# Kernel optimization log

Hardware: AMD Instinct MI355X
Metric: run time of the kernel (lower is better)

## Reference

```python
import jax, jax.numpy as jnp
import numpy as np

N1, N2, D = 2048, 2048, 64  # d_q_in=d_q_out=d_k_in=d_k_out=d_v=64


def setup_inputs() -> dict:
    key = jax.random.key(0)
    ks = jax.random.split(key, 9)
    s = 0.05
    return {
        "q": jax.random.normal(ks[0], (N1, D), dtype=jnp.float32),
        "k": jax.random.normal(ks[1], (N2, D), dtype=jnp.float32),
        "v": jax.random.normal(ks[2], (N2, D), dtype=jnp.float32),
        # q_w: Linear(d_q_in -> d_q_out)
        "Wq": jax.random.normal(ks[3], (D, D), dtype=jnp.float32) * s,
        "bq": jax.random.normal(ks[4], (D,), dtype=jnp.float32) * s,
        # k_w: Linear(d_k_in -> d_k_out)
        "Wk": jax.random.normal(ks[5], (D, D), dtype=jnp.float32) * s,
        "bk": jax.random.normal(ks[6], (D,), dtype=jnp.float32) * s,
        # w: Linear(d_q_out -> 1)
        "w": jax.random.normal(ks[7], (D,), dtype=jnp.float32) * s,
        "b": jax.random.normal(ks[8], (1,), dtype=jnp.float32) * s,
    }


def reference(q, k, v, Wq, bq, Wk, bk, w, b):
    # x' = w3 * sigma(w1*q + w2*k); Bahdanau-style additive attention.
    qp = q @ Wq + bq                      # [N1, D]
    kp = k @ Wk + bk                      # [N2, D]
    h = jax.nn.sigmoid(qp[:, None, :] + kp[None, :, :])   # [N1, N2, D]
    att_score = jnp.einsum("nmd,d->nm", h, w) + b[0]       # [N1, N2]
    att_weight = jax.nn.softmax(att_score, axis=-1)
    output = att_weight @ v               # [N1, D]
    return (output, att_score)
```

## Files before the change

### kernel.cpp

```cpp
#include <hip/hip_runtime.h>
#include <math.h>

#define N1 2048
#define N2 2048
#define DD 64
#define NJ 10
#define KDIM (DD*NJ)
#define NKS32 40

static constexpr float LOG2E = 1.4426950408889634f;
static constexpr float ACLIP = 2.6f;

typedef _Float16 f16x8  __attribute__((ext_vector_type(8)));
typedef float    f32x16 __attribute__((ext_vector_type(16)));
typedef float    v2f    __attribute__((ext_vector_type(2)));

__device__ const float XNODE_dev[NJ] = {
     2.5679897f,  2.3166170f,  1.8384776f,  1.1803753f,  0.4067296f,
    -0.4067296f, -1.1803753f, -1.8384776f, -2.3166170f, -2.5679897f };
__device__ const float WBAR_dev[NJ] = {
     1.4751660e-3f, -4.2811330e-3f,  6.6679880e-3f, -8.4021590e-3f,
     9.3138610e-3f, -9.3138610e-3f,  8.4021590e-3f, -6.6679880e-3f,
     4.2811330e-3f, -1.4751660e-3f };

__device__ __forceinline__ void gll16(const void* g, void* l) {
    __builtin_amdgcn_global_load_lds(
        (const __attribute__((address_space(1))) void*)g,
        (__attribute__((address_space(3))) void*)l,
        16, 0, 0);
}

__global__ __launch_bounds__(256) void k_prep(
    const float* __restrict__ q, const float* __restrict__ k,
    const float* __restrict__ Wq, const float* __restrict__ bq,
    const float* __restrict__ Wk, const float* __restrict__ bk,
    const float* __restrict__ w,
    f16x8* __restrict__ Ap, f16x8* __restrict__ Bp)
{
    int t = threadIdx.x;
    bool is_q = blockIdx.x < 64;
    int tile = is_q ? blockIdx.x : (blockIdx.x - 64);
    int row0 = tile * 32;
    const float* X    = is_q ? q : k;
    const float* W    = is_q ? Wq : Wk;
    const float* bias = is_q ? bq : bk;

    __shared__ float4 xs4[32][16];
    __shared__ float  pp[32][66];
    __shared__ float  wls[64];
    __shared__ float  xn_s[NJ], wb_s[NJ];

    #pragma unroll
    for (int s = 0; s < 2; ++s) {
        int slot = t + 256 * s;
        int r = slot >> 4, c4 = slot & 15;
        xs4[r][c4] = *(const float4*)&X[(row0 + r) * DD + c4 * 4];
    }
    if (t < 64) wls[t] = w[t];
    if (t >= 64 && t < 64 + NJ) xn_s[t - 64] = XNODE_dev[t - 64];
    if (t >= 96 && t < 96 + NJ) wb_s[t - 96] = WBAR_dev[t - 96];
    __syncthreads();

    {
        int col = t & 63, wvi = t >> 6;
        float acc[8];
        float bv = bias[col];
        #pragma unroll
        for (int i = 0; i < 8; ++i) acc[i] = bv;
        #pragma unroll
        for (int j4 = 0; j4 < 16; ++j4) {
            float wj[4];
            #pragma unroll
            for (int jj = 0; jj < 4; ++jj)
                wj[jj] = W[(j4 * 4 + jj) * DD + col];
            #pragma unroll
            for (int i = 0; i < 8; ++i) {
                float4 xv = xs4[wvi + 4 * i][j4];
                acc[i] = fmaf(xv.x, wj[0], acc[i]);
                acc[i] = fmaf(xv.y, wj[1], acc[i]);
                acc[i] = fmaf(xv.z, wj[2], acc[i]);
                acc[i] = fmaf(xv.w, wj[3], acc[i]);
            }
        }
        #pragma unroll
        for (int i = 0; i < 8; ++i)
            pp[wvi + 4 * i][col] = acc[i];
    }
    __syncthreads();

    #pragma unroll
    for (int s = 0; s < 10; ++s) {
        int slot = t + 256 * s;
        int ks = slot >> 6, lane = slot & 63;
        int row = lane & 31;
        int kbase = ks * 16 + (lane >> 5) * 8;
        f16x8 o;
        if (is_q) {
            #pragma unroll
            for (int jj = 0; jj < 8; ++jj) {
                int kk = kbase + jj;
                int d = (kk * 6554) >> 16;
                int j = kk - d * 10;
                float a = pp[row][d];
                a = fminf(fmaxf(a, -ACLIP), ACLIP);
                float p = wb_s[j];
                #pragma unroll
                for (int i = 0; i < NJ; ++i)
                    p *= (i == j) ? 1.0f : (a - xn_s[i]);
                o[jj] = (_Float16)(p * wls[d]);
            }
            Ap[(tile * NKS32 + ks) * 64 + lane] = o;
        } else {
            #pragma unroll
            for (int jj = 0; jj < 8; ++jj) {
                int kk = kbase + jj;
                int d = (kk * 6554) >> 16;
                int j = kk - d * 10;
                float sv = xn_s[j] + pp[row][d];
                float sg = __builtin_amdgcn_rcpf(
                    1.0f + __builtin_amdgcn_exp2f(-sv * LOG2E));
                o[jj] = (_Float16)sg;
            }
            Bp[(tile * NKS32 + ks) * 64 + lane] = o;
        }
    }
}

__global__ __launch_bounds__(256) void k_gemm(
    const f16x8* __restrict__ Ap, const f16x8* __restrict__ Bp,
    const float* __restrict__ bscal, float* __restrict__ score)
{
    int bx = blockIdx.x;
    int xcd = bx & 7;
    int sub = (bx >> 3) & 3;
    int mb  = bx >> 5;
    int nb  = xcd * 4 + sub;

    int t = threadIdx.x, wv = t >> 6, lane = t & 63;
    int ma = (wv >> 1) * 2;
    int nloc = wv & 1;

    __shared__ f16x8 sbuf[24][64];

    const int ST = NKS32 * 64;

    const f16x8* cbase[6];
    int ckl[6];
    #pragma unroll
    for (int j = 0; j < 6; ++j) {
        int cc = wv * 6 + j;
        int tile = cc >> 2;
        ckl[j] = cc & 3;
        cbase[j] = (tile < 4) ? (Ap + (mb * 4 + tile) * ST)
                              : (Bp + (nb * 2 + (tile - 4)) * ST);
    }

    f32x16 acc[2] = {};

    for (int it = 0; it < 10; ++it) {
        if (it) __syncthreads();
        #pragma unroll
        for (int j = 0; j < 6; ++j) {
            int cc = wv * 6 + j;
            gll16(cbase[j] + (it * 4 + ckl[j]) * 64 + lane, &sbuf[cc][0]);
        }
        __syncthreads();
        #pragma unroll
        for (int kl = 0; kl < 4; ++kl) {
            f16x8 a0 = sbuf[(ma + 0) * 4 + kl][lane];
            f16x8 a1 = sbuf[(ma + 1) * 4 + kl][lane];
            f16x8 b  = sbuf[(4 + nloc) * 4 + kl][lane];
            acc[0] = __builtin_amdgcn_mfma_f32_32x32x16_f16(a0, b, acc[0], 0, 0, 0);
            acc[1] = __builtin_amdgcn_mfma_f32_32x32x16_f16(a1, b, acc[1], 0, 0, 0);
        }
    }

    float bias = bscal[0];
    int nt0 = nb * 2 + nloc;
    int colg = nt0 * 32 + (lane & 31);
    #pragma unroll
    for (int i = 0; i < 2; ++i) {
        int rbase = (mb * 4 + ma + i) * 32 + 4 * (lane >> 5);
        #pragma unroll
        for (int r = 0; r < 16; ++r) {
            int rowg = rbase + (r & 3) + 8 * (r >> 2);
            score[rowg * N2 + colg] = acc[i][r] + bias;
        }
    }
}

__global__ __launch_bounds__(256) void k_out(
    const float* __restrict__ score, const float* __restrict__ v,
    float* __restrict__ out)
{
    int n0 = blockIdx.x * 4;
    __shared__ float p_lds[2][2048][2];
    __shared__ float red[4][4];
    __shared__ float part[4][4][64];
    __shared__ float inv_s[4];
    int t = threadIdx.x, wv = t >> 6, lane = t & 63;

    float psum[4];
    #pragma unroll
    for (int r = 0; r < 4; ++r) {
        psum[r] = 0.f;
        const float* srow = score + (n0 + r) * N2;
        #pragma unroll
        for (int kk = 0; kk < 8; ++kk) {
            int m = t + 256 * kk;
            float p = __builtin_amdgcn_exp2f(srow[m] * LOG2E);
            p_lds[r >> 1][m][r & 1] = p;
            psum[r] += p;
        }
    }
    #pragma unroll
    for (int r = 0; r < 4; ++r) {
        float x = psum[r];
        #pragma unroll
        for (int off = 32; off > 0; off >>= 1)
            x += __shfl_down(x, off, 64);
        if (lane == 0) red[r][wv] = x;
    }
    __syncthreads();
    if (t < 4)
        inv_s[t] = 1.0f / (red[t][0] + red[t][1] + red[t][2] + red[t][3]);
    __syncthreads();

    int m_off = lane >> 4, d4 = lane & 15;
    const float4* v4 = (const float4*)v;
    float4 a[4] = {{0,0,0,0},{0,0,0,0},{0,0,0,0},{0,0,0,0}};
    int mstart = wv * 512;
    #pragma unroll 4
    for (int i = 0; i < 128; ++i) {
        int m = mstart + i * 4 + m_off;
        v2f p01 = *(const v2f*)&p_lds[0][m][0];
        v2f p23 = *(const v2f*)&p_lds[1][m][0];
        float4 vv = v4[m * 16 + d4];
        a[0].x = fmaf(p01.x, vv.x, a[0].x);  a[0].y = fmaf(p01.x, vv.y, a[0].y);
        a[0].z = fmaf(p01.x, vv.z, a[0].z);  a[0].w = fmaf(p01.x, vv.w, a[0].w);
        a[1].x = fmaf(p01.y, vv.x, a[1].x);  a[1].y = fmaf(p01.y, vv.y, a[1].y);
        a[1].z = fmaf(p01.y, vv.z, a[1].z);  a[1].w = fmaf(p01.y, vv.w, a[1].w);
        a[2].x = fmaf(p23.x, vv.x, a[2].x);  a[2].y = fmaf(p23.x, vv.y, a[2].y);
        a[2].z = fmaf(p23.x, vv.z, a[2].z);  a[2].w = fmaf(p23.x, vv.w, a[2].w);
        a[3].x = fmaf(p23.y, vv.x, a[3].x);  a[3].y = fmaf(p23.y, vv.y, a[3].y);
        a[3].z = fmaf(p23.y, vv.z, a[3].z);  a[3].w = fmaf(p23.y, vv.w, a[3].w);
    }
    #pragma unroll
    for (int r = 0; r < 4; ++r) {
        #pragma unroll
        for (int off = 16; off <= 32; off <<= 1) {
            a[r].x += __shfl_xor(a[r].x, off, 64);
            a[r].y += __shfl_xor(a[r].y, off, 64);
            a[r].z += __shfl_xor(a[r].z, off, 64);
            a[r].w += __shfl_xor(a[r].w, off, 64);
        }
    }
    if (lane < 16) {
        #pragma unroll
        for (int r = 0; r < 4; ++r)
            *(float4*)&part[wv][r][d4 * 4] = a[r];
    }
    __syncthreads();
    {
        int r = t >> 6, d = t & 63;
        float s = part[0][r][d] + part[1][r][d] + part[2][r][d] + part[3][r][d];
        out[(n0 + r) * DD + d] = s * inv_s[r];
    }
}

__global__ __launch_bounds__(256) void k_proj_old(
    const float* __restrict__ q, const float* __restrict__ k,
    const float* __restrict__ Wq, const float* __restrict__ bq,
    const float* __restrict__ Wk, const float* __restrict__ bk,
    float* __restrict__ qp, float* __restrict__ kpT)
{
    int bx = blockIdx.x;
    bool is_q = bx < 512;
    int row0 = (is_q ? bx : bx - 512) * 4;
    const float* X = is_q ? q : k;
    const float* W = is_q ? Wq : Wk;
    const float* bias = is_q ? bq : bk;

    __shared__ float xrow[4][64];
    int t = threadIdx.x;
    int wv = t >> 6, lane = t & 63;
    xrow[wv][lane] = X[(row0 + wv) * DD + lane];
    __syncthreads();

    float acc = 0.f;
    #pragma unroll
    for (int j = 0; j < 64; ++j)
        acc = fmaf(xrow[wv][j], W[j * DD + lane], acc);

    float val = -(acc + bias[lane]) * LOG2E;
    int row = row0 + wv;
    if (is_q) qp[row * DD + lane] = val;
    else      kpT[lane * N2 + row] = val;
}

__global__ __launch_bounds__(256, 8) void k_score_old(
    const float* __restrict__ qp, const float* __restrict__ kpT,
    const float* __restrict__ w, const float* __restrict__ b,
    float* __restrict__ score)
{
    int bx = blockIdx.x;
    int n0 = (bx >> 3) * 8;
    int m_base = (bx & 7) * 256;

    __shared__ float qp_s[8][64];
    __shared__ float w_s[64];
    int t = threadIdx.x;
    if (t < 128)
        ((float4*)qp_s)[t] = ((const float4*)(qp + n0 * DD))[t];
    if (t < 64) w_s[t] = w[t];
    float b0 = b[0];
    __syncthreads();

    int rgrp = t >> 6, lane = t & 63;
    int r0 = rgrp * 2;
    int m0 = m_base + lane * 4;

    float acc[2][4];
    #pragma unroll
    for (int i2 = 0; i2 < 2; ++i2)
        #pragma unroll
        for (int j = 0; j < 4; ++j)
            acc[i2][j] = b0;

    const float* kbase = kpT + m0;

    for (int d0 = 0; d0 < 64; d0 += 4) {
        float4 kv[4];
        #pragma unroll
        for (int dd = 0; dd < 4; ++dd)
            kv[dd] = *(const float4*)(kbase + (d0 + dd) * N2);

        float4 wvv = *(const float4*)&w_s[d0];
        #pragma unroll
        for (int i2 = 0; i2 < 2; ++i2) {
            float4 qv = *(const float4*)&qp_s[r0 + i2][d0];
            #pragma unroll
            for (int dd = 0; dd < 4; ++dd) {
                float qvd = (&qv.x)[dd];
                float wd  = (&wvv.x)[dd];
                #pragma unroll
                for (int j = 0; j < 4; ++j) {
                    float x = qvd + (&kv[dd].x)[j];
                    float e = __builtin_amdgcn_exp2f(x);
                    float sg = __builtin_amdgcn_rcpf(1.0f + e);
                    acc[i2][j] = fmaf(wd, sg, acc[i2][j]);
                }
            }
        }
    }

    #pragma unroll
    for (int i2 = 0; i2 < 2; ++i2) {
        float4 o = { acc[i2][0], acc[i2][1], acc[i2][2], acc[i2][3] };
        *(float4*)&score[(n0 + r0 + i2) * N2 + m0] = o;
    }
}

extern "C" void kernel_launch(void* const* d_in, const int* in_sizes, int n_in,
                              void* d_out, int out_size, void* d_ws, size_t ws_size,
                              hipStream_t stream) {
    const float* q  = (const float*)d_in[0];
    const float* k  = (const float*)d_in[1];
    const float* v  = (const float*)d_in[2];
    const float* Wq = (const float*)d_in[3];
    const float* bq = (const float*)d_in[4];
    const float* Wk = (const float*)d_in[5];
    const float* bk = (const float*)d_in[6];
    const float* w  = (const float*)d_in[7];
    const float* b  = (const float*)d_in[8];

    float* out   = (float*)d_out;
    float* score = out + N1 * DD;

    const size_t PACKED = (size_t)2048 * KDIM * 2;

    if (ws_size >= 2 * PACKED) {
        f16x8* Ap = (f16x8*)d_ws;
        f16x8* Bp = (f16x8*)((char*)d_ws + PACKED);

        k_prep<<<128, 256, 0, stream>>>(q, k, Wq, bq, Wk, bk, w, Ap, Bp);
        k_gemm<<<512, 256, 0, stream>>>(Ap, Bp, b, score);
        k_out <<<512, 256, 0, stream>>>(score, v, out);
    } else {
        float* qp  = (float*)d_ws;
        float* kpT = qp + N1 * DD;
        k_proj_old <<<1024, 256, 0, stream>>>(q, k, Wq, bq, Wk, bk, qp, kpT);
        k_score_old<<<2048, 256, 0, stream>>>(qp, kpT, w, b, score);
        k_out      <<<512, 256, 0, stream>>>(score, v, out);
    }
}
```

Baseline: 115.7 us.

## Fuse softmax and PV into score GEMM, cut interpolation nodes to 8

The polynomial interpolation of the sigmoid drops from 10 to 8 nodes, which shrinks the GEMM K dimension from 640 to 512 and replaces the divide-by-10 indexing with shifts. The score GEMM epilogue now computes exp of each score tile into LDS and accumulates row sums with atomics. It then multiplies that tile by a pre-packed fp16 V in MFMA and writes per-column-block fp16 partial outputs. A small normalization kernel sums the 32 partials and divides by the row sum, replacing the separate k_out pass that re-read the full score matrix. The softmax skips max subtraction, relying on the scores staying small, and fp16 partials and fewer nodes both reduce accuracy.

```diff
diff --git a/kernel.cpp b/kernel.cpp
--- a/kernel.cpp
+++ b/kernel.cpp
@@ -4,24 +4,25 @@
 #define N1 2048
 #define N2 2048
 #define DD 64
-#define NJ 10
+#define NJ 8
 #define KDIM (DD*NJ)
-#define NKS32 40
+#define NKS32 (KDIM/16)
 
 static constexpr float LOG2E = 1.4426950408889634f;
 static constexpr float ACLIP = 2.6f;
 
 typedef _Float16 f16x8  __attribute__((ext_vector_type(8)));
+typedef _Float16 h2     __attribute__((ext_vector_type(2)));
+typedef _Float16 h4     __attribute__((ext_vector_type(4)));
 typedef float    f32x16 __attribute__((ext_vector_type(16)));
 typedef float    v2f    __attribute__((ext_vector_type(2)));
 
 __device__ const float XNODE_dev[NJ] = {
-     2.5679897f,  2.3166170f,  1.8384776f,  1.1803753f,  0.4067296f,
-    -0.4067296f, -1.1803753f, -1.8384776f, -2.3166170f, -2.5679897f };
+     2.5500417f,  2.1618210f,  1.4444826f,  0.5072348f,
+    -0.5072348f, -1.4444826f, -2.1618210f, -2.5500417f };
 __device__ const float WBAR_dev[NJ] = {
-     1.4751660e-3f, -4.2811330e-3f,  6.6679880e-3f, -8.4021590e-3f,
-     9.3138610e-3f, -9.3138610e-3f,  8.4021590e-3f, -6.6679880e-3f,
-     4.2811330e-3f, -1.4751660e-3f };
+     3.886344e-3f, -1.1067395e-2f,  1.6563510e-2f, -1.9538005e-2f,
+     1.9538005e-2f, -1.6563510e-2f,  1.1067395e-2f, -3.886344e-3f };
 
 __device__ __forceinline__ void gll16(const void* g, void* l) {
     __builtin_amdgcn_global_load_lds(
@@ -32,14 +33,43 @@
 
 __global__ __launch_bounds__(256) void k_prep(
     const float* __restrict__ q, const float* __restrict__ k,
+    const float* __restrict__ v,
     const float* __restrict__ Wq, const float* __restrict__ bq,
     const float* __restrict__ Wk, const float* __restrict__ bk,
     const float* __restrict__ w,
-    f16x8* __restrict__ Ap, f16x8* __restrict__ Bp)
+    f16x8* __restrict__ Ap, f16x8* __restrict__ Bp,
+    f16x8* __restrict__ Vp, float* __restrict__ rowsum)
 {
     int t = threadIdx.x;
-    bool is_q = blockIdx.x < 64;
-    int tile = is_q ? blockIdx.x : (blockIdx.x - 64);
+    int bx = blockIdx.x;
+
+    if (bx >= 144) {
+        #pragma unroll
+        for (int i = 0; i < 8; ++i) rowsum[t + 256 * i] = 0.f;
+        return;
+    }
+    if (bx >= 128) {
+        int vb = bx - 128;
+        #pragma unroll
+        for (int s = 0; s < 4; ++s) {
+            int slot = t + 256 * s;
+            int dtile = slot >> 9;
+            int ksl = (slot >> 6) & 7;
+            int lane = slot & 63;
+            int ksg = vb * 8 + ksl;
+            int d = dtile * 32 + (lane & 31);
+            int mbase = ksg * 16 + (lane >> 5) * 8;
+            f16x8 o;
+            #pragma unroll
+            for (int jj = 0; jj < 8; ++jj)
+                o[jj] = (_Float16)v[(mbase + jj) * DD + d];
+            Vp[(dtile * 128 + ksg) * 64 + lane] = o;
+        }
+        return;
+    }
+
+    bool is_q = bx < 64;
+    int tile = is_q ? bx : (bx - 64);
     int row0 = tile * 32;
     const float* X    = is_q ? q : k;
     const float* W    = is_q ? Wq : Wk;
@@ -89,7 +119,7 @@
     __syncthreads();
 
     #pragma unroll
-    for (int s = 0; s < 10; ++s) {
+    for (int s = 0; s < 8; ++s) {
         int slot = t + 256 * s;
         int ks = slot >> 6, lane = slot & 63;
         int row = lane & 31;
@@ -99,8 +129,7 @@
             #pragma unroll
             for (int jj = 0; jj < 8; ++jj) {
                 int kk = kbase + jj;
-                int d = (kk * 6554) >> 16;
-                int j = kk - d * 10;
+                int d = kk >> 3, j = kk & 7;
                 float a = pp[row][d];
                 a = fminf(fmaxf(a, -ACLIP), ACLIP);
                 float p = wb_s[j];
@@ -114,8 +143,7 @@
             #pragma unroll
             for (int jj = 0; jj < 8; ++jj) {
                 int kk = kbase + jj;
-                int d = (kk * 6554) >> 16;
-                int j = kk - d * 10;
+                int d = kk >> 3, j = kk & 7;
                 float sv = xn_s[j] + pp[row][d];
                 float sg = __builtin_amdgcn_rcpf(
                     1.0f + __builtin_amdgcn_exp2f(-sv * LOG2E));
@@ -128,7 +156,9 @@
 
 __global__ __launch_bounds__(256) void k_gemm(
     const f16x8* __restrict__ Ap, const f16x8* __restrict__ Bp,
-    const float* __restrict__ bscal, float* __restrict__ score)
+    const f16x8* __restrict__ Vp, const float* __restrict__ bscal,
+    float* __restrict__ score, _Float16* __restrict__ part,
+    float* __restrict__ rowsum)
 {
     int bx = blockIdx.x;
     int xcd = bx & 7;
@@ -141,7 +171,6 @@
     int nloc = wv & 1;
 
     __shared__ f16x8 sbuf[24][64];
-
     const int ST = NKS32 * 64;
 
     const f16x8* cbase[6];
@@ -157,13 +186,12 @@
 
     f32x16 acc[2] = {};
 
-    for (int it = 0; it < 10; ++it) {
+    for (int it = 0; it < 8; ++it) {
         if (it) __syncthreads();
         #pragma unroll
-        for (int j = 0; j < 6; ++j) {
-            int cc = wv * 6 + j;
-            gll16(cbase[j] + (it * 4 + ckl[j]) * 64 + lane, &sbuf[cc][0]);
-        }
+        for (int j = 0; j < 6; ++j)
+            gll16(cbase[j] + (it * 4 + ckl[j]) * 64 + lane,
+                  &sbuf[wv * 6 + j][0]);
         __syncthreads();
         #pragma unroll
         for (int kl = 0; kl < 4; ++kl) {
@@ -175,21 +203,178 @@
         }
     }
 
+    __syncthreads();
+    _Float16* Pl = (_Float16*)&sbuf[0][0];
+
     float bias = bscal[0];
-    int nt0 = nb * 2 + nloc;
-    int colg = nt0 * 32 + (lane & 31);
+    int colL = nloc * 32 + (lane & 31);
+    int colG = (nb * 2 + nloc) * 32 + (lane & 31);
     #pragma unroll
     for (int i = 0; i < 2; ++i) {
-        int rbase = (mb * 4 + ma + i) * 32 + 4 * (lane >> 5);
+        int rbaseL = (ma + i) * 32 + 4 * (lane >> 5);
+        int rbaseG = mb * 128 + rbaseL;
         #pragma unroll
         for (int r = 0; r < 16; ++r) {
-            int rowg = rbase + (r & 3) + 8 * (r >> 2);
-            score[rowg * N2 + colg] = acc[i][r] + bias;
-        }
-    }
-}
-
-__global__ __launch_bounds__(256) void k_out(
+            int ro = (r & 3) + 8 * (r >> 2);
+            float s = acc[i][r] + bias;
+            score[(rbaseG + ro) * N2 + colG] = s;
+            Pl[(rbaseL + ro) * 72 + colL] =
+                (_Float16)__builtin_amdgcn_exp2f(s * LOG2E);
+        }
+    }
+    __syncthreads();
+
+    {
+        int row = t >> 1, hf = t & 1;
+        const h2* pr = (const h2*)Pl;
+        float rs = 0.f;
+        #pragma unroll
+        for (int u = 0; u < 16; ++u) {
+            h2 pv = pr[row * 36 + hf * 16 + u];
+            rs += (float)pv[0] + (float)pv[1];
+        }
+        atomicAdd(&rowsum[mb * 128 + row], rs);
+    }
+
+    {
+        f32x16 oacc[2] = {};
+        const f16x8* pv0 = Vp + (0 * 128 + nb * 4) * 64 + lane;
+        const f16x8* pv1 = Vp + (1 * 128 + nb * 4) * 64 + lane;
+        #pragma unroll
+        for (int ks = 0; ks < 4; ++ks) {
+            f16x8 af = *(const f16x8*)&Pl[(wv * 32 + (lane & 31)) * 72
+                                          + ks * 16 + (lane >> 5) * 8];
+            f16x8 b0 = pv0[ks * 64];
+            f16x8 b1 = pv1[ks * 64];
+            oacc[0] = __builtin_amdgcn_mfma_f32_32x32x16_f16(af, b0, oacc[0], 0, 0, 0);
+            oacc[1] = __builtin_amdgcn_mfma_f32_32x32x16_f16(af, b1, oacc[1], 0, 0, 0);
+        }
+        #pragma unroll
+        for (int dt = 0; dt < 2; ++dt) {
+            int d = dt * 32 + (lane & 31);
+            int nbase = mb * 128 + wv * 32 + 4 * (lane >> 5);
+            #pragma unroll
+            for (int r = 0; r < 16; ++r) {
+                int nG = nbase + (r & 3) + 8 * (r >> 2);
+                part[(nb * 2048 + nG) * 64 + d] = (_Float16)oacc[dt][r];
+            }
+        }
+    }
+}
+
+__global__ __launch_bounds__(256) void k_norm(
+    const _Float16* __restrict__ part, const float* __restrict__ rowsum,
+    float* __restrict__ out)
+{
+    int gid = blockIdx.x * 256 + threadIdx.x;
+    int n = gid >> 4;
+    int dq = (gid & 15) * 4;
+    float s0 = 0.f, s1 = 0.f, s2 = 0.f, s3 = 0.f;
+    #pragma unroll 8
+    for (int nb = 0; nb < 32; ++nb) {
+        h4 pv = *(const h4*)&part[(nb * 2048 + n) * 64 + dq];
+        s0 += (float)pv[0]; s1 += (float)pv[1];
+        s2 += (float)pv[2]; s3 += (float)pv[3];
+    }
+    float inv = __builtin_amdgcn_rcpf(rowsum[n]);
+    float4 o = { s0 * inv, s1 * inv, s2 * inv, s3 * inv };
+    *(float4*)&out[n * DD + dq] = o;
+}
+
+__global__ __launch_bounds__(256) void k_proj_old(
+    const float* __restrict__ q, const float* __restrict__ k,
+    const float* __restrict__ Wq, const float* __restrict__ bq,
+    const float* __restrict__ Wk, const float* __restrict__ bk,
+    float* __restrict__ qp, float* __restrict__ kpT)
+{
+    int bx = blockIdx.x;
+    bool is_q = bx < 512;
+    int row0 = (is_q ? bx : bx - 512) * 4;
+    const float* X = is_q ? q : k;
+    const float* W = is_q ? Wq : Wk;
+    const float* bias = is_q ? bq : bk;
+
+    __shared__ float xrow[4][64];
+    int t = threadIdx.x;
+    int wv = t >> 6, lane = t & 63;
+    xrow[wv][lane] = X[(row0 + wv) * DD + lane];
+    __syncthreads();
+
+    float acc = 0.f;
+    #pragma unroll
+    for (int j = 0; j < 64; ++j)
+        acc = fmaf(xrow[wv][j], W[j * DD + lane], acc);
+
+    float val = -(acc + bias[lane]) * LOG2E;
+    int row = row0 + wv;
+    if (is_q) qp[row * DD + lane] = val;
+    else      kpT[lane * N2 + row] = val;
+}
+
+__global__ __launch_bounds__(256, 8) void k_score_old(
+    const float* __restrict__ qp, const float* __restrict__ kpT,
+    const float* __restrict__ w, const float* __restrict__ b,
+    float* __restrict__ score)
+{
+    int bx = blockIdx.x;
+    int n0 = (bx >> 3) * 8;
+    int m_base = (bx & 7) * 256;
+
+    __shared__ float qp_s[8][64];
+    __shared__ float w_s[64];
+    int t = threadIdx.x;
+    if (t < 128)
+        ((float4*)qp_s)[t] = ((const float4*)(qp + n0 * DD))[t];
+    if (t < 64) w_s[t] = w[t];
+    float b0 = b[0];
+    __syncthreads();
+
+    int rgrp = t >> 6, lane = t & 63;
+    int r0 = rgrp * 2;
+    int m0 = m_base + lane * 4;
+
+    float acc[2][4];
+    #pragma unroll
+    for (int i2 = 0; i2 < 2; ++i2)
+        #pragma unroll
+        for (int j = 0; j < 4; ++j)
+            acc[i2][j] = b0;
+
+    const float* kbase = kpT + m0;
+
+    for (int d0 = 0; d0 < 64; d0 += 4) {
+        float4 kv[4];
+        #pragma unroll
+        for (int dd = 0; dd < 4; ++dd)
+            kv[dd] = *(const float4*)(kbase + (d0 + dd) * N2);
+
+        float4 wvv = *(const float4*)&w_s[d0];
+        #pragma unroll
+        for (int i2 = 0; i2 < 2; ++i2) {
+            float4 qv = *(const float4*)&qp_s[r0 + i2][d0];
+            #pragma unroll
+            for (int dd = 0; dd < 4; ++dd) {
+                float qvd = (&qv.x)[dd];
+                float wd  = (&wvv.x)[dd];
+                #pragma unroll
+                for (int j = 0; j < 4; ++j) {
+                    float x = qvd + (&kv[dd].x)[j];
+                    float e = __builtin_amdgcn_exp2f(x);
+                    float sg = __builtin_amdgcn_rcpf(1.0f + e);
+                    acc[i2][j] = fmaf(wd, sg, acc[i2][j]);
+                }
+            }
+        }
+    }
+
+    #pragma unroll
+    for (int i2 = 0; i2 < 2; ++i2) {
+        float4 o = { acc[i2][0], acc[i2][1], acc[i2][2], acc[i2][3] };
+        *(float4*)&score[(n0 + r0 + i2) * N2 + m0] = o;
+    }
+}
+
+__global__ __launch_bounds__(256) void k_out_old(
     const float* __restrict__ score, const float* __restrict__ v,
     float* __restrict__ out)
 {
@@ -268,99 +453,6 @@
     }
 }
 
-__global__ __launch_bounds__(256) void k_proj_old(
-    const float* __restrict__ q, const float* __restrict__ k,
-    const float* __restrict__ Wq, const float* __restrict__ bq,
-    const float* __restrict__ Wk, const float* __restrict__ bk,
-    float* __restrict__ qp, float* __restrict__ kpT)
-{
-    int bx = blockIdx.x;
-    bool is_q = bx < 512;
-    int row0 = (is_q ? bx : bx - 512) * 4;
-    const float* X = is_q ? q : k;
-    const float* W = is_q ? Wq : Wk;
-    const float* bias = is_q ? bq : bk;
-
-    __shared__ float xrow[4][64];
-    int t = threadIdx.x;
-    int wv = t >> 6, lane = t & 63;
-    xrow[wv][lane] = X[(row0 + wv) * DD + lane];
-    __syncthreads();
-
-    float acc = 0.f;
-    #pragma unroll
-    for (int j = 0; j < 64; ++j)
-        acc = fmaf(xrow[wv][j], W[j * DD + lane], acc);
-
-    float val = -(acc + bias[lane]) * LOG2E;
-    int row = row0 + wv;
-    if (is_q) qp[row * DD + lane] = val;
-    else      kpT[lane * N2 + row] = val;
-}
-
-__global__ __launch_bounds__(256, 8) void k_score_old(
-    const float* __restrict__ qp, const float* __restrict__ kpT,
-    const float* __restrict__ w, const float* __restrict__ b,
-    float* __restrict__ score)
-{
-    int bx = blockIdx.x;
-    int n0 = (bx >> 3) * 8;
-    int m_base = (bx & 7) * 256;
-
-    __shared__ float qp_s[8][64];
-    __shared__ float w_s[64];
-    int t = threadIdx.x;
-    if (t < 128)
-        ((float4*)qp_s)[t] = ((const float4*)(qp + n0 * DD))[t];
-    if (t < 64) w_s[t] = w[t];
-    float b0 = b[0];
-    __syncthreads();
-
-    int rgrp = t >> 6, lane = t & 63;
-    int r0 = rgrp * 2;
-    int m0 = m_base + lane * 4;
-
-    float acc[2][4];
-    #pragma unroll
-    for (int i2 = 0; i2 < 2; ++i2)
-        #pragma unroll
-        for (int j = 0; j < 4; ++j)
-            acc[i2][j] = b0;
-
-    const float* kbase = kpT + m0;
-
-    for (int d0 = 0; d0 < 64; d0 += 4) {
-        float4 kv[4];
-        #pragma unroll
-        for (int dd = 0; dd < 4; ++dd)
-            kv[dd] = *(const float4*)(kbase + (d0 + dd) * N2);
-
-        float4 wvv = *(const float4*)&w_s[d0];
-        #pragma unroll
-        for (int i2 = 0; i2 < 2; ++i2) {
-            float4 qv = *(const float4*)&qp_s[r0 + i2][d0];
-            #pragma unroll
-            for (int dd = 0; dd < 4; ++dd) {
-                float qvd = (&qv.x)[dd];
-                float wd  = (&wvv.x)[dd];
-                #pragma unroll
-                for (int j = 0; j < 4; ++j) {
-                    float x = qvd + (&kv[dd].x)[j];
-                    float e = __builtin_amdgcn_exp2f(x);
-                    float sg = __builtin_amdgcn_rcpf(1.0f + e);
-                    acc[i2][j] = fmaf(wd, sg, acc[i2][j]);
-                }
-            }
-        }
-    }
-
-    #pragma unroll
-    for (int i2 = 0; i2 < 2; ++i2) {
-        float4 o = { acc[i2][0], acc[i2][1], acc[i2][2], acc[i2][3] };
-        *(float4*)&score[(n0 + r0 + i2) * N2 + m0] = o;
-    }
-}
-
 extern "C" void kernel_launch(void* const* d_in, const int* in_sizes, int n_in,
                               void* d_out, int out_size, void* d_ws, size_t ws_size,
                               hipStream_t stream) {
@@ -377,20 +469,29 @@
     float* out   = (float*)d_out;
     float* score = out + N1 * DD;
 
-    const size_t PACKED = (size_t)2048 * KDIM * 2;
-
-    if (ws_size >= 2 * PACKED) {
-        f16x8* Ap = (f16x8*)d_ws;
-        f16x8* Bp = (f16x8*)((char*)d_ws + PACKED);
-
-        k_prep<<<128, 256, 0, stream>>>(q, k, Wq, bq, Wk, bk, w, Ap, Bp);
-        k_gemm<<<512, 256, 0, stream>>>(Ap, Bp, b, score);
-        k_out <<<512, 256, 0, stream>>>(score, v, out);
+    const size_t SZ_AB  = (size_t)2048 * KDIM * 2;
+    const size_t SZ_VP  = (size_t)2048 * DD * 2;
+    const size_t SZ_RS  = 2048 * 4;
+    const size_t SZ_PT  = (size_t)32 * 2048 * DD * 2;
+    const size_t NEED   = 2 * SZ_AB + SZ_VP + SZ_RS + SZ_PT;
+
+    if (ws_size >= NEED) {
+        char* p = (char*)d_ws;
+        f16x8*    Ap = (f16x8*)p;                 p += SZ_AB;
+        f16x8*    Bp = (f16x8*)p;                 p += SZ_AB;
+        f16x8*    Vp = (f16x8*)p;                 p += SZ_VP;
+        float*    rowsum = (float*)p;             p += SZ_RS;
+        _Float16* part = (_Float16*)p;
+
+        k_prep<<<145, 256, 0, stream>>>(q, k, v, Wq, bq, Wk, bk, w,
+                                        Ap, Bp, Vp, rowsum);
+        k_gemm<<<512, 256, 0, stream>>>(Ap, Bp, Vp, b, score, part, rowsum);
+        k_norm<<<128, 256, 0, stream>>>(part, rowsum, out);
     } else {
         float* qp  = (float*)d_ws;
         float* kpT = qp + N1 * DD;
         k_proj_old <<<1024, 256, 0, stream>>>(q, k, Wq, bq, Wk, bk, qp, kpT);
         k_score_old<<<2048, 256, 0, stream>>>(qp, kpT, w, b, score);
-        k_out      <<<512, 256, 0, stream>>>(score, v, out);
-    }
-}
+        k_out_old  <<<512, 256, 0, stream>>>(score, v, out);
+    }
+}
```

Result: faster. 109.8 us (-5.1%).
